# Kernel tuning notes

Measured on AMD Instinct MI355X. Metric: run time of the kernel, lower is better.

The kernel has to match this reference:

```python
import jax, jax.numpy as jnp
import numpy as np

D_MODEL = 256
NHEAD = 8
HEAD_DIM = D_MODEL // NHEAD
TOP_K = 16
TEMP = 0.1
INF = 1e9
LAYER_NAMES = ['self', 'cross'] * 4


def _ln(x, g, b):
    m = jnp.mean(x, -1, keepdims=True)
    v = jnp.mean((x - m) ** 2, -1, keepdims=True)
    return (x - m) * jax.lax.rsqrt(v + 1e-5) * g + b


def _conf(f0, f1, m0, m1):
    # feats scaled by 1/sqrt(C) each, then /temperature -> sim / (C * TEMP)
    c = f0.shape[-1]
    sim = jnp.einsum('nlc,nsc->nls', f0, f1) / (c * TEMP)
    valid = m0[:, :, None] & m1[:, None, :]
    sim = jnp.where(valid, sim, -INF)
    return jax.nn.softmax(sim, axis=1) * jax.nn.softmax(sim, axis=2)


def _select(feat, conf, k):
    _, idx = jax.lax.top_k(conf, k)                 # [N, L, K]
    return jax.vmap(lambda f, i: f[i])(feat, idx)    # [N, L, K, C]


def _lin_attn(q, k, v, qm):
    # LoFTR LinearAttention: elu feature map, kv_mask is None here
    Q = jax.nn.elu(q) + 1.0
    K = jax.nn.elu(k) + 1.0
    if qm is not None:
        Q = Q * qm[:, :, None, None]
    vlen = v.shape[1]
    v = v / vlen
    KV = jnp.einsum('nshd,nshv->nhdv', K, v)
    Z = 1.0 / (jnp.einsum('nlhd,nhd->nlh', Q, K.sum(1)) + 1e-6)
    return jnp.einsum('nlhd,nhdv,nlh->nlhv', Q, KV, Z) * vlen


def _layer(x, src, xm, p):
    Wq, Wk, Wv, Wm, W1, W2, g1, b1, g2, b2 = p
    bs = x.shape[0]
    q = (x @ Wq).reshape(bs, -1, NHEAD, HEAD_DIM)
    k = (src @ Wk).reshape(bs, -1, NHEAD, HEAD_DIM)
    v = (src @ Wv).reshape(bs, -1, NHEAD, HEAD_DIM)
    msg = _lin_attn(q, k, v, xm)
    msg = msg.reshape(bs, -1, D_MODEL) @ Wm
    msg = _ln(msg, g1, b1)
    msg = jax.nn.relu(jnp.concatenate([x, msg], -1) @ W1) @ W2
    msg = _ln(msg, g2, b2)
    return x + msg


def _forward(feat0, feat1, mask0, mask1, Wq, Wk, Wv, Wm, W1, W2, g1, b1, g2, b2):
    N, L, C = feat0.shape
    S = feat1.shape[1]
    K = TOP_K
    m0f = mask0.reshape(N * L, 1).astype(feat0.dtype)
    m1f = mask1.reshape(N * S, 1).astype(feat0.dtype)
    for i, name in enumerate(LAYER_NAMES):
        p = (Wq[i], Wk[i], Wv[i], Wm[i], W1[i], W2[i], g1[i], b1[i], g2[i], b2[i])
        f0 = feat0.reshape(N * L, 1, C)
        f1 = feat1.reshape(N * S, 1, C)
        if name == 'self':
            s00 = _select(feat0, _conf(feat0, feat0, mask0, mask0), K).reshape(N * L, K, C)
            s11 = _select(feat1, _conf(feat1, feat1, mask1, mask1), K).reshape(N * S, K, C)
            feat0 = _layer(f0, s00, m0f, p).reshape(N, L, C)
            feat1 = _layer(f1, s11, m1f, p).reshape(N, S, C)
        else:
            c01 = _conf(feat0, feat1, mask0, mask1)
            s01 = _select(feat1, c01, K).reshape(N * L, K, C)
            s10 = _select(feat0, jnp.swapaxes(c01, 1, 2), K).reshape(N * S, K, C)
            feat0 = _layer(f0, s01, m0f, p).reshape(N, L, C)
            feat1 = _layer(f1, s10, m1f, p).reshape(N, S, C)
    return feat0, feat1


def setup_inputs() -> dict:
    key = jax.random.key(0)
    ks = jax.random.split(key, 10)
    N, L, S, C = 2, 4800, 4800, D_MODEL
    nl = len(LAYER_NAMES)
    w = 0.05
    return {
        'feat0': jax.random.normal(ks[0], (N, L, C), jnp.float32),
        'feat1': jax.random.normal(ks[1], (N, S, C), jnp.float32),
        'mask0': jnp.ones((N, L), jnp.bool_),
        'mask1': jnp.ones((N, S), jnp.bool_),
        'Wq': jax.random.normal(ks[2], (nl, C, C), jnp.float32) * w,
        'Wk': jax.random.normal(ks[3], (nl, C, C), jnp.float32) * w,
        'Wv': jax.random.normal(ks[4], (nl, C, C), jnp.float32) * w,
        'Wm': jax.random.normal(ks[5], (nl, C, C), jnp.float32) * w,
        'W1': jax.random.normal(ks[6], (nl, 2 * C, 2 * C), jnp.float32) * w,
        'W2': jax.random.normal(ks[7], (nl, 2 * C, C), jnp.float32) * w,
        'g1': jnp.ones((nl, C), jnp.float32),
        'b1': jnp.zeros((nl, C), jnp.float32),
        'g2': jnp.ones((nl, C), jnp.float32),
        'b2': jnp.zeros((nl, C), jnp.float32),
    }


def reference(feat0, feat1, mask0, mask1, Wq, Wk, Wv, Wm, W1, W2, g1, b1, g2, b2):
    return _forward(feat0, feat1, mask0, mask1, Wq, Wk, Wv, Wm, W1, W2, g1, b1, g2, b2)
```

## Files before the change

### kernel.cpp

```cpp
#include <hip/hip_runtime.h>

#define LLEN 4800
#define CDIM 256
#define NCH 8
#define CHROWS 600
#define SUBR 75

template <int MODE>
__global__ __launch_bounds__(256) void gemm_nt_sim(
    const float* __restrict__ A, const float* __restrict__ B,
    float* __restrict__ C, float* __restrict__ CT)
{
  const int bxi = blockIdx.x, byi = blockIdx.y;
  if (MODE == 1 && bxi < byi) return;
  const int bm = byi * 128, bn = bxi * 128;
  __shared__ float pool[MODE ? 8512 : 4224];
  float (*As)[132] = (float (*)[132])pool;
  float (*Bs)[132] = (float (*)[132])(pool + 2112);
  const int t = threadIdx.x;
  const int tx = t & 15, ty = t >> 4;
  const int lr = t >> 2, lk = (t & 3) * 4;
  float acc[8][8] = {};
  for (int k0 = 0; k0 < CDIM; k0 += 16) {
#pragma unroll
    for (int h = 0; h < 2; ++h) {
      const int row = lr + h * 64;
      const int ga = min(bm + row, LLEN - 1);
      const int gb = min(bn + row, LLEN - 1);
      const float4 a = *(const float4*)&A[(size_t)ga * CDIM + k0 + lk];
      const float4 b = *(const float4*)&B[(size_t)gb * CDIM + k0 + lk];
      As[lk + 0][row] = a.x; As[lk + 1][row] = a.y;
      As[lk + 2][row] = a.z; As[lk + 3][row] = a.w;
      Bs[lk + 0][row] = b.x; Bs[lk + 1][row] = b.y;
      Bs[lk + 2][row] = b.z; Bs[lk + 3][row] = b.w;
    }
    __syncthreads();
#pragma unroll
    for (int k = 0; k < 16; ++k) {
      const float4 a0 = *(const float4*)&As[k][ty * 4];
      const float4 a1 = *(const float4*)&As[k][64 + ty * 4];
      const float4 b0 = *(const float4*)&Bs[k][tx * 4];
      const float4 b1 = *(const float4*)&Bs[k][64 + tx * 4];
      const float av[8] = {a0.x, a0.y, a0.z, a0.w, a1.x, a1.y, a1.z, a1.w};
      const float bv[8] = {b0.x, b0.y, b0.z, b0.w, b1.x, b1.y, b1.z, b1.w};
#pragma unroll
      for (int i = 0; i < 8; ++i)
#pragma unroll
        for (int j = 0; j < 8; ++j) acc[i][j] += av[i] * bv[j];
    }
    __syncthreads();
  }
  const float sc = 1.f / 25.6f;
#pragma unroll
  for (int i = 0; i < 8; ++i) {
    const int row = bm + ((i < 4) ? ty * 4 + i : 64 + ty * 4 + (i - 4));
    if (row < LLEN) {
      const int c0 = bn + tx * 4;
      if (c0 < LLEN) {
        float4 o = {acc[i][0] * sc, acc[i][1] * sc, acc[i][2] * sc, acc[i][3] * sc};
        *(float4*)(C + (size_t)row * LLEN + c0) = o;
      }
      if (c0 + 64 < LLEN) {
        float4 o = {acc[i][4] * sc, acc[i][5] * sc, acc[i][6] * sc, acc[i][7] * sc};
        *(float4*)(C + (size_t)row * LLEN + c0 + 64) = o;
      }
    }
  }
  if (MODE == 0) return;
  if (MODE == 1 && bxi == byi) return;
  float* D = (MODE == 1) ? C : CT;
  float (*Ts)[133] = (float (*)[133])pool;
  for (int chunk = 0; chunk < 2; ++chunk) {
    __syncthreads();
#pragma unroll
    for (int i = 0; i < 8; ++i) {
      const int rl = (i < 4) ? ty * 4 + i : 64 + ty * 4 + (i - 4);
#pragma unroll
      for (int jj = 0; jj < 4; ++jj)
        Ts[tx * 4 + jj][rl] = acc[i][chunk * 4 + jj] * sc;
    }
    __syncthreads();
    const int cl = t >> 2, seg = t & 3;
    const int drow = bn + chunk * 64 + cl;
    if (drow < LLEN) {
#pragma unroll
      for (int q = 0; q < 8; ++q) {
        const int dcol = bm + seg * 32 + q * 4;
        if (dcol < LLEN) {
          const int b = seg * 32 + q * 4;
          float4 o = {Ts[cl][b], Ts[cl][b + 1], Ts[cl][b + 2], Ts[cl][b + 3]};
          *(float4*)(D + (size_t)drow * LLEN + dcol) = o;
        }
      }
    }
  }
}

template <int ACT>
__global__ __launch_bounds__(256) void gemm_nn(
    const float* __restrict__ A1, const float* __restrict__ A2,
    const float* __restrict__ B, float* __restrict__ C, int N, int K, int KA1)
{
  const int bm = blockIdx.y * 128, bn = blockIdx.x * 128;
  __shared__ float As[16][132];
  __shared__ float Bs[16][132];
  const int t = threadIdx.x;
  const int tx = t & 15, ty = t >> 4;
  const int lr = t >> 2, lk = (t & 3) * 4;
  const int bc = (t & 31) * 4, bk = t >> 5;
  float acc[8][8] = {};
  for (int k0 = 0; k0 < K; k0 += 16) {
    const float* Ap; int kloc, lda;
    if (k0 < KA1) { Ap = A1; kloc = k0; lda = KA1; }
    else          { Ap = A2; kloc = k0 - KA1; lda = K - KA1; }
#pragma unroll
    for (int h = 0; h < 2; ++h) {
      const int row = lr + h * 64;
      const float4 a = *(const float4*)&Ap[(size_t)(bm + row) * lda + kloc + lk];
      As[lk + 0][row] = a.x; As[lk + 1][row] = a.y;
      As[lk + 2][row] = a.z; As[lk + 3][row] = a.w;
    }
#pragma unroll
    for (int h = 0; h < 2; ++h) {
      const int kr = bk + h * 8;
      *(float4*)&Bs[kr][bc] = *(const float4*)&B[(size_t)(k0 + kr) * N + bn + bc];
    }
    __syncthreads();
#pragma unroll
    for (int k = 0; k < 16; ++k) {
      const float4 a0 = *(const float4*)&As[k][ty * 4];
      const float4 a1 = *(const float4*)&As[k][64 + ty * 4];
      const float4 b0 = *(const float4*)&Bs[k][tx * 4];
      const float4 b1 = *(const float4*)&Bs[k][64 + tx * 4];
      const float av[8] = {a0.x, a0.y, a0.z, a0.w, a1.x, a1.y, a1.z, a1.w};
      const float bv[8] = {b0.x, b0.y, b0.z, b0.w, b1.x, b1.y, b1.z, b1.w};
#pragma unroll
      for (int i = 0; i < 8; ++i)
#pragma unroll
        for (int j = 0; j < 8; ++j) acc[i][j] += av[i] * bv[j];
    }
    __syncthreads();
  }
#pragma unroll
  for (int i = 0; i < 8; ++i) {
    const int row = bm + ((i < 4) ? ty * 4 + i : 64 + ty * 4 + (i - 4));
    float4 o0 = {acc[i][0], acc[i][1], acc[i][2], acc[i][3]};
    float4 o1 = {acc[i][4], acc[i][5], acc[i][6], acc[i][7]};
    if (ACT == 1) {
      o0.x = fmaxf(o0.x, 0.f); o0.y = fmaxf(o0.y, 0.f);
      o0.z = fmaxf(o0.z, 0.f); o0.w = fmaxf(o0.w, 0.f);
      o1.x = fmaxf(o1.x, 0.f); o1.y = fmaxf(o1.y, 0.f);
      o1.z = fmaxf(o1.z, 0.f); o1.w = fmaxf(o1.w, 0.f);
    }
    *(float4*)(C + (size_t)row * N + bn + tx * 4) = o0;
    *(float4*)(C + (size_t)row * N + bn + tx * 4 + 64) = o1;
  }
}

__global__ __launch_bounds__(256) void gemm_qkv(
    const float* __restrict__ F,
    const float* __restrict__ Wq, const float* __restrict__ Wk, const float* __restrict__ Wv,
    float* __restrict__ qb, float* __restrict__ kb, float* __restrict__ vb)
{
  const int bm = blockIdx.y * 128;
  const int gn = blockIdx.x * 128;
  const int sel = gn >> 8;
  const int bn = gn & 255;
  const float* __restrict__ B = (sel == 0) ? Wq : (sel == 1) ? Wk : Wv;
  float* __restrict__ C = (sel == 0) ? qb : (sel == 1) ? kb : vb;
  __shared__ float As[16][132];
  __shared__ float Bs[16][132];
  const int t = threadIdx.x;
  const int tx = t & 15, ty = t >> 4;
  const int lr = t >> 2, lk = (t & 3) * 4;
  const int bc = (t & 31) * 4, bk = t >> 5;
  float acc[8][8] = {};
  for (int k0 = 0; k0 < CDIM; k0 += 16) {
#pragma unroll
    for (int h = 0; h < 2; ++h) {
      const int row = lr + h * 64;
      const float4 a = *(const float4*)&F[(size_t)(bm + row) * CDIM + k0 + lk];
      As[lk + 0][row] = a.x; As[lk + 1][row] = a.y;
      As[lk + 2][row] = a.z; As[lk + 3][row] = a.w;
    }
#pragma unroll
    for (int h = 0; h < 2; ++h) {
      const int kr = bk + h * 8;
      *(float4*)&Bs[kr][bc] = *(const float4*)&B[(size_t)(k0 + kr) * CDIM + bn + bc];
    }
    __syncthreads();
#pragma unroll
    for (int k = 0; k < 16; ++k) {
      const float4 a0 = *(const float4*)&As[k][ty * 4];
      const float4 a1 = *(const float4*)&As[k][64 + ty * 4];
      const float4 b0 = *(const float4*)&Bs[k][tx * 4];
      const float4 b1 = *(const float4*)&Bs[k][64 + tx * 4];
      const float av[8] = {a0.x, a0.y, a0.z, a0.w, a1.x, a1.y, a1.z, a1.w};
      const float bv[8] = {b0.x, b0.y, b0.z, b0.w, b1.x, b1.y, b1.z, b1.w};
#pragma unroll
      for (int i = 0; i < 8; ++i)
#pragma unroll
        for (int j = 0; j < 8; ++j) acc[i][j] += av[i] * bv[j];
    }
    __syncthreads();
  }
#pragma unroll
  for (int i = 0; i < 8; ++i) {
    const int row = bm + ((i < 4) ? ty * 4 + i : 64 + ty * 4 + (i - 4));
    float4 o0 = {acc[i][0], acc[i][1], acc[i][2], acc[i][3]};
    float4 o1 = {acc[i][4], acc[i][5], acc[i][6], acc[i][7]};
    *(float4*)(C + (size_t)row * CDIM + bn + tx * 4) = o0;
    *(float4*)(C + (size_t)row * CDIM + bn + tx * 4 + 64) = o1;
  }
}

__global__ __launch_bounds__(256) void row_stats(
    const float* __restrict__ sim, float* __restrict__ rowAdj)
{
  const int r = blockIdx.x;
  const float* row = sim + (size_t)r * LLEN;
  const int t = threadIdx.x;
  float m = -3e38f, s = 0.f;
  for (int j = t; j < LLEN; j += 256) {
    float x = row[j];
    if (x > m) { s = s * __expf(m - x) + 1.f; m = x; }
    else s += __expf(x - m);
  }
  __shared__ float sMax[256];
  __shared__ float sSum[256];
  sMax[t] = m; sSum[t] = s;
  __syncthreads();
  for (int off = 128; off > 0; off >>= 1) {
    if (t < off) {
      float m2 = sMax[t + off], s2 = sSum[t + off];
      float mm = fmaxf(sMax[t], m2);
      sSum[t] = sSum[t] * __expf(sMax[t] - mm) + s2 * __expf(m2 - mm);
      sMax[t] = mm;
    }
    __syncthreads();
  }
  if (t == 0) rowAdj[r] = sMax[0] + __logf(sSum[0]);
}

__global__ __launch_bounds__(256) void col_stats(
    const float* __restrict__ sim, float* __restrict__ partM, float* __restrict__ partS)
{
  const int t = threadIdx.x;
  const int c = t & 31, sub = t >> 5;
  const int s = blockIdx.x * 32 + c;
  const int ch = blockIdx.y;
  float m = -3e38f, sum = 0.f;
  const int l0 = ch * CHROWS + sub * SUBR;
  for (int l = l0; l < l0 + SUBR; ++l) {
    const float x = sim[(size_t)l * LLEN + s];
    if (x > m) { sum = sum * __expf(m - x) + 1.f; m = x; }
    else sum += __expf(x - m);
  }
  __shared__ float lm[8][32];
  __shared__ float ls[8][32];
  lm[sub][c] = m; ls[sub][c] = sum;
  __syncthreads();
  if (sub == 0) {
    float M = -3e38f, S = 0.f;
#pragma unroll
    for (int u = 0; u < 8; ++u) {
      const float m2 = lm[u][c], s2 = ls[u][c];
      const float mm = fmaxf(M, m2);
      S = S * __expf(M - mm) + s2 * __expf(m2 - mm);
      M = mm;
    }
    partM[(size_t)ch * LLEN + s] = M;
    partS[(size_t)ch * LLEN + s] = S;
  }
}

__global__ __launch_bounds__(256) void col_comb_stats(
    const float* __restrict__ partM, const float* __restrict__ partS,
    float* __restrict__ colAdj)
{
  const int s = blockIdx.x * 256 + threadIdx.x;
  if (s >= LLEN) return;
  float m = -3e38f, sum = 0.f;
#pragma unroll
  for (int ch = 0; ch < NCH; ++ch) {
    const float m2 = partM[(size_t)ch * LLEN + s], s2 = partS[(size_t)ch * LLEN + s];
    const float mm = fmaxf(m, m2);
    sum = sum * __expf(m - mm) + s2 * __expf(m2 - mm);
    m = mm;
  }
  colAdj[s] = m + __logf(sum);
}

__global__ __launch_bounds__(256, 4) void topk_fast(
    const float* __restrict__ M, const float* __restrict__ adj,
    int* __restrict__ idxOut, int kvOff)
{
  const int r = blockIdx.x;
  const float* row = M + (size_t)r * LLEN;
  const int t = threadIdx.x, lane = t & 63, w = t >> 6;
  __shared__ float keys[256 * 19];
  float lm = -3e38f; int la = 0;
#pragma unroll
  for (int j = 0; j < 19; ++j) {
    const int s = t + (j << 8);
    const float k = (s < LLEN) ? 2.f * row[s] - adj[s] : -3e38f;
    keys[t * 19 + j] = k;
    if (k > lm) { lm = k; la = j; }
  }
  __shared__ float wvv[4][16];
  __shared__ int   wii[4][16];
  for (int rnd = 0; rnd < 16; ++rnd) {
    float bv = lm;
    int   bs = (la << 8) + t;
#pragma unroll
    for (int off = 32; off; off >>= 1) {
      const float ov = __shfl_xor(bv, off);
      const int   os = __shfl_xor(bs, off);
      if (ov > bv || (ov == bv && os < bs)) { bv = ov; bs = os; }
    }
    if (lane == 0) { wvv[w][rnd] = bv; wii[w][rnd] = bs; }
    if (t == (bs & 255)) {
      keys[t * 19 + (bs >> 8)] = -3e38f;
      lm = -3e38f; la = 0;
#pragma unroll
      for (int j = 0; j < 19; ++j) {
        const float k = keys[t * 19 + j];
        if (k > lm) { lm = k; la = j; }
      }
    }
  }
  __syncthreads();
  if (w == 0) {
    float v = wvv[lane >> 4][lane & 15];
    const int s = wii[lane >> 4][lane & 15];
    for (int rnd = 0; rnd < 16; ++rnd) {
      float bv = v; int bl = lane;
#pragma unroll
      for (int off = 32; off; off >>= 1) {
        const float ov = __shfl_xor(bv, off);
        const int   ol = __shfl_xor(bl, off);
        if (ov > bv || (ov == bv && ol < bl)) { bv = ov; bl = ol; }
      }
      const int sw = __shfl(s, bl);
      if (lane == 0) idxOut[(size_t)r * 16 + rnd] = kvOff + sw;
      if (lane == bl) v = -3e38f;
    }
  }
}

__global__ __launch_bounds__(256) void attn_kernel(
    float* __restrict__ qb, const float* __restrict__ kb,
    const float* __restrict__ vb, const int* __restrict__ idx, int nTok)
{
  const int w = threadIdx.x >> 6, lane = threadIdx.x & 63;
  const int tok = blockIdx.x * 4 + w;
  if (tok >= nTok) return;
  const float4 qv = ((const float4*)(qb + (size_t)tok * CDIM))[lane];
  float Q[4];
  Q[0] = qv.x > 0.f ? qv.x + 1.f : __expf(qv.x);
  Q[1] = qv.y > 0.f ? qv.y + 1.f : __expf(qv.y);
  Q[2] = qv.z > 0.f ? qv.z + 1.f : __expf(qv.z);
  Q[3] = qv.w > 0.f ? qv.w + 1.f : __expf(qv.w);
  const int* ir = idx + (size_t)tok * 16;
  float mc[4] = {0.f, 0.f, 0.f, 0.f};
  float z = 0.f;
  for (int j = 0; j < 16; ++j) {
    const int src = ir[j];
    const float4 kv = ((const float4*)(kb + (size_t)src * CDIM))[lane];
    float p = Q[0] * (kv.x > 0.f ? kv.x + 1.f : __expf(kv.x))
            + Q[1] * (kv.y > 0.f ? kv.y + 1.f : __expf(kv.y))
            + Q[2] * (kv.z > 0.f ? kv.z + 1.f : __expf(kv.z))
            + Q[3] * (kv.w > 0.f ? kv.w + 1.f : __expf(kv.w));
    p += __shfl_xor(p, 1);
    p += __shfl_xor(p, 2);
    p += __shfl_xor(p, 4);
    const float4 vv = ((const float4*)(vb + (size_t)src * CDIM))[lane];
    mc[0] += p * vv.x; mc[1] += p * vv.y; mc[2] += p * vv.z; mc[3] += p * vv.w;
    z += p;
  }
  const float Z = 1.f / (z + 1e-6f);
  float4 o;
  o.x = mc[0] * Z; o.y = mc[1] * Z; o.z = mc[2] * Z; o.w = mc[3] * Z;
  ((float4*)(qb + (size_t)tok * CDIM))[lane] = o;
}

__global__ __launch_bounds__(256) void ln_inplace(
    float* __restrict__ x, const float* __restrict__ g, const float* __restrict__ b,
    int rows)
{
  const int w = threadIdx.x >> 6, lane = threadIdx.x & 63;
  const int r = blockIdx.x * 4 + w;
  if (r >= rows) return;
  float4 v = ((const float4*)(x + (size_t)r * CDIM))[lane];
  float s = v.x + v.y + v.z + v.w;
  float ss = v.x * v.x + v.y * v.y + v.z * v.z + v.w * v.w;
#pragma unroll
  for (int off = 1; off < 64; off <<= 1) {
    s += __shfl_xor(s, off);
    ss += __shfl_xor(ss, off);
  }
  const float mean = s * (1.f / CDIM);
  const float var = ss * (1.f / CDIM) - mean * mean;
  const float rstd = rsqrtf(var + 1e-5f);
  const float4 gv = ((const float4*)g)[lane];
  const float4 bv = ((const float4*)b)[lane];
  float4 o;
  o.x = (v.x - mean) * rstd * gv.x + bv.x;
  o.y = (v.y - mean) * rstd * gv.y + bv.y;
  o.z = (v.z - mean) * rstd * gv.z + bv.z;
  o.w = (v.w - mean) * rstd * gv.w + bv.w;
  ((float4*)(x + (size_t)r * CDIM))[lane] = o;
}

__global__ __launch_bounds__(256) void ln_res_kernel(
    const float* __restrict__ m2, const float* __restrict__ xin,
    const float* __restrict__ g, const float* __restrict__ b,
    float* __restrict__ out, int rows)
{
  const int w = threadIdx.x >> 6, lane = threadIdx.x & 63;
  const int r = blockIdx.x * 4 + w;
  if (r >= rows) return;
  const float4 v = ((const float4*)(m2 + (size_t)r * CDIM))[lane];
  float s = v.x + v.y + v.z + v.w;
  float ss = v.x * v.x + v.y * v.y + v.z * v.z + v.w * v.w;
#pragma unroll
  for (int off = 1; off < 64; off <<= 1) {
    s += __shfl_xor(s, off);
    ss += __shfl_xor(ss, off);
  }
  const float mean = s * (1.f / CDIM);
  const float var = ss * (1.f / CDIM) - mean * mean;
  const float rstd = rsqrtf(var + 1e-5f);
  const float4 gv = ((const float4*)g)[lane];
  const float4 bv = ((const float4*)b)[lane];
  const float4 xv = ((const float4*)(xin + (size_t)r * CDIM))[lane];
  float4 o;
  o.x = xv.x + (v.x - mean) * rstd * gv.x + bv.x;
  o.y = xv.y + (v.y - mean) * rstd * gv.y + bv.y;
  o.z = xv.z + (v.z - mean) * rstd * gv.z + bv.z;
  o.w = xv.w + (v.w - mean) * rstd * gv.w + bv.w;
  ((float4*)(out + (size_t)r * CDIM))[lane] = o;
}

extern "C" void kernel_launch(void* const* d_in, const int* in_sizes, int n_in,
                              void* d_out, int out_size, void* d_ws, size_t ws_size,
                              hipStream_t stream)
{
  (void)in_sizes; (void)n_in; (void)out_size;
  const float* in0 = (const float*)d_in[0];
  const float* in1 = (const float*)d_in[1];
  const float* Wq = (const float*)d_in[4];
  const float* Wk = (const float*)d_in[5];
  const float* Wv = (const float*)d_in[6];
  const float* Wm = (const float*)d_in[7];
  const float* W1 = (const float*)d_in[8];
  const float* W2 = (const float*)d_in[9];
  const float* g1 = (const float*)d_in[10];
  const float* b1 = (const float*)d_in[11];
  const float* g2 = (const float*)d_in[12];
  const float* b2 = (const float*)d_in[13];

  const size_t SIMF   = (size_t)LLEN * LLEN;
  const size_t SIDEQ  = (size_t)9600 * CDIM;
  const size_t NEED_F = SIMF + 4800 + 4800 + 2 * (size_t)NCH * LLEN
                      + 2 * (size_t)NCH * LLEN * 16 + (size_t)19200 * 16;
  if (ws_size < NEED_F * sizeof(float)) return;
  const bool haveT = (ws_size >= (NEED_F + SIMF) * sizeof(float));

  float* ws = (float*)d_ws;
  float* sim    = ws;
  float* rowAdj = ws + SIMF;
  float* colAdj = rowAdj + 4800;
  float* partM  = colAdj + 4800;
  float* partS  = partM + (size_t)NCH * LLEN;
  float* candV  = partS + (size_t)NCH * LLEN;
  int*   idxb   = (int*)(candV + 2 * (size_t)NCH * LLEN * 16);
  float* simT   = ws + NEED_F;

  float* qb = sim;
  float* kb = sim + 2 * SIDEQ;
  float* vb = sim + 4 * SIDEQ;
  float* hb = sim + 6 * SIDEQ;
  float* m2 = kb;
  float* mw = vb;

  const size_t fstride = (size_t)LLEN * CDIM;
  float* fA0 = (float*)d_out;
  float* fA1 = (float*)d_out + 2 * fstride;

  const float* cF0 = in0;
  const float* cF1 = in1;

  for (int i = 0; i < 8; ++i) {
    const bool isSelf = ((i & 1) == 0);
    const float* Wq_i = Wq + (size_t)i * CDIM * CDIM;
    const float* Wk_i = Wk + (size_t)i * CDIM * CDIM;
    const float* Wv_i = Wv + (size_t)i * CDIM * CDIM;
    const float* Wm_i = Wm + (size_t)i * CDIM * CDIM;
    const float* W1_i = W1 + (size_t)i * 512 * 512;
    const float* W2_i = W2 + (size_t)i * 512 * CDIM;
    const float* g1_i = g1 + (size_t)i * CDIM;
    const float* b1_i = b1 + (size_t)i * CDIM;
    const float* g2_i = g2 + (size_t)i * CDIM;
    const float* b2_i = b2 + (size_t)i * CDIM;

    if (isSelf) {
      for (int side = 0; side < 2; ++side) {
        const float* F = side ? cF1 : cF0;
        for (int n = 0; n < 2; ++n) {
          const float* Fn = F + (size_t)n * fstride;
          gemm_nt_sim<1><<<dim3(38, 38), 256, 0, stream>>>(Fn, Fn, sim, sim);
          row_stats<<<LLEN, 256, 0, stream>>>(sim, rowAdj);
          topk_fast<<<LLEN, 256, 0, stream>>>(
              sim, rowAdj, idxb + ((size_t)side * 9600 + (size_t)n * LLEN) * 16,
              side * 9600 + n * LLEN);
        }
      }
    } else {
      for (int n = 0; n < 2; ++n) {
        const float* F0n = cF0 + (size_t)n * fstride;
        const float* F1n = cF1 + (size_t)n * fstride;
        if (haveT) {
          gemm_nt_sim<2><<<dim3(38, 38), 256, 0, stream>>>(F0n, F1n, sim, simT);
          row_stats<<<LLEN, 256, 0, stream>>>(sim, rowAdj);
          col_stats<<<dim3(150, NCH), 256, 0, stream>>>(sim, partM, partS);
          col_comb_stats<<<dim3(19), 256, 0, stream>>>(partM, partS, colAdj);
          topk_fast<<<LLEN, 256, 0, stream>>>(
              sim, colAdj, idxb + ((size_t)n * LLEN) * 16, 9600 + n * LLEN);
          topk_fast<<<LLEN, 256, 0, stream>>>(
              simT, rowAdj, idxb + ((size_t)9600 + (size_t)n * LLEN) * 16, n * LLEN);
        } else {
          gemm_nt_sim<0><<<dim3(38, 38), 256, 0, stream>>>(F0n, F1n, sim, nullptr);
          row_stats<<<LLEN, 256, 0, stream>>>(sim, rowAdj);
          col_stats<<<dim3(150, NCH), 256, 0, stream>>>(sim, partM, partS);
          col_comb_stats<<<dim3(19), 256, 0, stream>>>(partM, partS, colAdj);
          topk_fast<<<LLEN, 256, 0, stream>>>(
              sim, colAdj, idxb + ((size_t)n * LLEN) * 16, 9600 + n * LLEN);
          gemm_nt_sim<0><<<dim3(38, 38), 256, 0, stream>>>(F1n, F0n, sim, nullptr);
          topk_fast<<<LLEN, 256, 0, stream>>>(
              sim, rowAdj, idxb + ((size_t)9600 + (size_t)n * LLEN) * 16, n * LLEN);
        }
      }
    }

    for (int side = 0; side < 2; ++side) {
      const float* F = side ? cF1 : cF0;
      const size_t ob = (size_t)side * SIDEQ;
      gemm_qkv<<<dim3(6, 75), 256, 0, stream>>>(
          F, Wq_i, Wk_i, Wv_i, qb + ob, kb + ob, vb + ob);
    }

    for (int side = 0; side < 2; ++side)
      attn_kernel<<<2400, 256, 0, stream>>>(
          qb + side * SIDEQ, kb, vb, idxb + (size_t)side * 9600 * 16, 9600);

    for (int side = 0; side < 2; ++side)
      gemm_nn<0><<<dim3(2, 75), 256, 0, stream>>>(
          qb + side * SIDEQ, nullptr, Wm_i, mw + side * SIDEQ, 256, 256, 256);
    ln_inplace<<<4800, 256, 0, stream>>>(mw, g1_i, b1_i, 19200);

    for (int side = 0; side < 2; ++side) {
      const float* F = side ? cF1 : cF0;
      gemm_nn<1><<<dim3(4, 75), 256, 0, stream>>>(
          F, mw + side * SIDEQ, W1_i, hb, 512, 512, 256);
      gemm_nn<0><<<dim3(2, 75), 256, 0, stream>>>(
          hb, nullptr, W2_i, m2 + side * SIDEQ, 256, 512, 512);
    }

    ln_res_kernel<<<2400, 256, 0, stream>>>(m2, cF0, g2_i, b2_i, fA0, 9600);
    ln_res_kernel<<<2400, 256, 0, stream>>>(m2 + SIDEQ, cF1, g2_i, b2_i, fA1, 9600);
    cF0 = fA0; cF1 = fA1;
  }
}
```

Baseline: 11.26 ms.

## Prefetch next K-tile in GEMMs, vectorize col_stats, merge per-side launches

The three register-tiled GEMM kernels now load the next 16-wide K slice from global memory into registers while the current slice is computed from shared memory, hiding global load latency behind the FMA loop. col_stats processes four columns per thread with float4 loads and 128-thread blocks. The per-side attention and Wm projection launches are merged into single launches over both sides, assuming contiguous buffers and an index layout that the larger indexing matches. The prefetch adds register pressure, and the merged launches depend on that buffer contiguity.

```diff
diff --git a/kernel.cpp b/kernel.cpp
--- a/kernel.cpp
+++ b/kernel.cpp
@@ -20,21 +20,31 @@
   const int t = threadIdx.x;
   const int tx = t & 15, ty = t >> 4;
   const int lr = t >> 2, lk = (t & 3) * 4;
+  const int ga0 = min(bm + lr, LLEN - 1)      , gb0 = min(bn + lr, LLEN - 1);
+  const int ga1 = min(bm + lr + 64, LLEN - 1) , gb1 = min(bn + lr + 64, LLEN - 1);
   float acc[8][8] = {};
+  float4 pa0, pa1, pb0, pb1;
+  pa0 = *(const float4*)&A[(size_t)ga0 * CDIM + lk];
+  pa1 = *(const float4*)&A[(size_t)ga1 * CDIM + lk];
+  pb0 = *(const float4*)&B[(size_t)gb0 * CDIM + lk];
+  pb1 = *(const float4*)&B[(size_t)gb1 * CDIM + lk];
   for (int k0 = 0; k0 < CDIM; k0 += 16) {
-#pragma unroll
-    for (int h = 0; h < 2; ++h) {
-      const int row = lr + h * 64;
-      const int ga = min(bm + row, LLEN - 1);
-      const int gb = min(bn + row, LLEN - 1);
-      const float4 a = *(const float4*)&A[(size_t)ga * CDIM + k0 + lk];
-      const float4 b = *(const float4*)&B[(size_t)gb * CDIM + k0 + lk];
-      As[lk + 0][row] = a.x; As[lk + 1][row] = a.y;
-      As[lk + 2][row] = a.z; As[lk + 3][row] = a.w;
-      Bs[lk + 0][row] = b.x; Bs[lk + 1][row] = b.y;
-      Bs[lk + 2][row] = b.z; Bs[lk + 3][row] = b.w;
-    }
-    __syncthreads();
+    As[lk + 0][lr] = pa0.x; As[lk + 1][lr] = pa0.y;
+    As[lk + 2][lr] = pa0.z; As[lk + 3][lr] = pa0.w;
+    As[lk + 0][lr + 64] = pa1.x; As[lk + 1][lr + 64] = pa1.y;
+    As[lk + 2][lr + 64] = pa1.z; As[lk + 3][lr + 64] = pa1.w;
+    Bs[lk + 0][lr] = pb0.x; Bs[lk + 1][lr] = pb0.y;
+    Bs[lk + 2][lr] = pb0.z; Bs[lk + 3][lr] = pb0.w;
+    Bs[lk + 0][lr + 64] = pb1.x; Bs[lk + 1][lr + 64] = pb1.y;
+    Bs[lk + 2][lr + 64] = pb1.z; Bs[lk + 3][lr + 64] = pb1.w;
+    __syncthreads();
+    if (k0 + 16 < CDIM) {
+      const int kn = k0 + 16 + lk;
+      pa0 = *(const float4*)&A[(size_t)ga0 * CDIM + kn];
+      pa1 = *(const float4*)&A[(size_t)ga1 * CDIM + kn];
+      pb0 = *(const float4*)&B[(size_t)gb0 * CDIM + kn];
+      pb1 = *(const float4*)&B[(size_t)gb1 * CDIM + kn];
+    }
 #pragma unroll
     for (int k = 0; k < 16; ++k) {
       const float4 a0 = *(const float4*)&As[k][ty * 4];
@@ -109,23 +119,32 @@
   const int lr = t >> 2, lk = (t & 3) * 4;
   const int bc = (t & 31) * 4, bk = t >> 5;
   float acc[8][8] = {};
+  float4 pa0, pa1, pb0, pb1;
+  {
+    const float* Ap = A1; const int kloc = 0, lda = KA1;
+    pa0 = *(const float4*)&Ap[(size_t)(bm + lr) * lda + kloc + lk];
+    pa1 = *(const float4*)&Ap[(size_t)(bm + lr + 64) * lda + kloc + lk];
+    pb0 = *(const float4*)&B[(size_t)(bk) * N + bn + bc];
+    pb1 = *(const float4*)&B[(size_t)(bk + 8) * N + bn + bc];
+  }
   for (int k0 = 0; k0 < K; k0 += 16) {
-    const float* Ap; int kloc, lda;
-    if (k0 < KA1) { Ap = A1; kloc = k0; lda = KA1; }
-    else          { Ap = A2; kloc = k0 - KA1; lda = K - KA1; }
-#pragma unroll
-    for (int h = 0; h < 2; ++h) {
-      const int row = lr + h * 64;
-      const float4 a = *(const float4*)&Ap[(size_t)(bm + row) * lda + kloc + lk];
-      As[lk + 0][row] = a.x; As[lk + 1][row] = a.y;
-      As[lk + 2][row] = a.z; As[lk + 3][row] = a.w;
-    }
-#pragma unroll
-    for (int h = 0; h < 2; ++h) {
-      const int kr = bk + h * 8;
-      *(float4*)&Bs[kr][bc] = *(const float4*)&B[(size_t)(k0 + kr) * N + bn + bc];
-    }
-    __syncthreads();
+    As[lk + 0][lr] = pa0.x; As[lk + 1][lr] = pa0.y;
+    As[lk + 2][lr] = pa0.z; As[lk + 3][lr] = pa0.w;
+    As[lk + 0][lr + 64] = pa1.x; As[lk + 1][lr + 64] = pa1.y;
+    As[lk + 2][lr + 64] = pa1.z; As[lk + 3][lr + 64] = pa1.w;
+    *(float4*)&Bs[bk][bc] = pb0;
+    *(float4*)&Bs[bk + 8][bc] = pb1;
+    __syncthreads();
+    const int kn = k0 + 16;
+    if (kn < K) {
+      const float* Ap; int kloc, lda;
+      if (kn < KA1) { Ap = A1; kloc = kn; lda = KA1; }
+      else          { Ap = A2; kloc = kn - KA1; lda = K - KA1; }
+      pa0 = *(const float4*)&Ap[(size_t)(bm + lr) * lda + kloc + lk];
+      pa1 = *(const float4*)&Ap[(size_t)(bm + lr + 64) * lda + kloc + lk];
+      pb0 = *(const float4*)&B[(size_t)(kn + bk) * N + bn + bc];
+      pb1 = *(const float4*)&B[(size_t)(kn + bk + 8) * N + bn + bc];
+    }
 #pragma unroll
     for (int k = 0; k < 16; ++k) {
       const float4 a0 = *(const float4*)&As[k][ty * 4];
@@ -175,20 +194,26 @@
   const int lr = t >> 2, lk = (t & 3) * 4;
   const int bc = (t & 31) * 4, bk = t >> 5;
   float acc[8][8] = {};
+  float4 pa0, pa1, pb0, pb1;
+  pa0 = *(const float4*)&F[(size_t)(bm + lr) * CDIM + lk];
+  pa1 = *(const float4*)&F[(size_t)(bm + lr + 64) * CDIM + lk];
+  pb0 = *(const float4*)&B[(size_t)(bk) * CDIM + bn + bc];
+  pb1 = *(const float4*)&B[(size_t)(bk + 8) * CDIM + bn + bc];
   for (int k0 = 0; k0 < CDIM; k0 += 16) {
-#pragma unroll
-    for (int h = 0; h < 2; ++h) {
-      const int row = lr + h * 64;
-      const float4 a = *(const float4*)&F[(size_t)(bm + row) * CDIM + k0 + lk];
-      As[lk + 0][row] = a.x; As[lk + 1][row] = a.y;
-      As[lk + 2][row] = a.z; As[lk + 3][row] = a.w;
-    }
-#pragma unroll
-    for (int h = 0; h < 2; ++h) {
-      const int kr = bk + h * 8;
-      *(float4*)&Bs[kr][bc] = *(const float4*)&B[(size_t)(k0 + kr) * CDIM + bn + bc];
-    }
-    __syncthreads();
+    As[lk + 0][lr] = pa0.x; As[lk + 1][lr] = pa0.y;
+    As[lk + 2][lr] = pa0.z; As[lk + 3][lr] = pa0.w;
+    As[lk + 0][lr + 64] = pa1.x; As[lk + 1][lr + 64] = pa1.y;
+    As[lk + 2][lr + 64] = pa1.z; As[lk + 3][lr + 64] = pa1.w;
+    *(float4*)&Bs[bk][bc] = pb0;
+    *(float4*)&Bs[bk + 8][bc] = pb1;
+    __syncthreads();
+    const int kn = k0 + 16;
+    if (kn < CDIM) {
+      pa0 = *(const float4*)&F[(size_t)(bm + lr) * CDIM + kn + lk];
+      pa1 = *(const float4*)&F[(size_t)(bm + lr + 64) * CDIM + kn + lk];
+      pb0 = *(const float4*)&B[(size_t)(kn + bk) * CDIM + bn + bc];
+      pb1 = *(const float4*)&B[(size_t)(kn + bk + 8) * CDIM + bn + bc];
+    }
 #pragma unroll
     for (int k = 0; k < 16; ++k) {
       const float4 a0 = *(const float4*)&As[k][ty * 4];
@@ -242,35 +267,45 @@
   if (t == 0) rowAdj[r] = sMax[0] + __logf(sSum[0]);
 }
 
-__global__ __launch_bounds__(256) void col_stats(
+__global__ __launch_bounds__(128) void col_stats(
     const float* __restrict__ sim, float* __restrict__ partM, float* __restrict__ partS)
 {
   const int t = threadIdx.x;
-  const int c = t & 31, sub = t >> 5;
-  const int s = blockIdx.x * 32 + c;
+  const int cg = t & 15, sub = t >> 4;
+  const int c0 = blockIdx.x * 64 + cg * 4;
   const int ch = blockIdx.y;
-  float m = -3e38f, sum = 0.f;
+  float m0 = -3e38f, m1 = -3e38f, m2 = -3e38f, m3 = -3e38f;
+  float s0 = 0.f, s1 = 0.f, s2 = 0.f, s3 = 0.f;
   const int l0 = ch * CHROWS + sub * SUBR;
   for (int l = l0; l < l0 + SUBR; ++l) {
-    const float x = sim[(size_t)l * LLEN + s];
-    if (x > m) { sum = sum * __expf(m - x) + 1.f; m = x; }
-    else sum += __expf(x - m);
-  }
-  __shared__ float lm[8][32];
-  __shared__ float ls[8][32];
-  lm[sub][c] = m; ls[sub][c] = sum;
+    const float4 x = *(const float4*)&sim[(size_t)l * LLEN + c0];
+    if (x.x > m0) { s0 = s0 * __expf(m0 - x.x) + 1.f; m0 = x.x; } else s0 += __expf(x.x - m0);
+    if (x.y > m1) { s1 = s1 * __expf(m1 - x.y) + 1.f; m1 = x.y; } else s1 += __expf(x.y - m1);
+    if (x.z > m2) { s2 = s2 * __expf(m2 - x.z) + 1.f; m2 = x.z; } else s2 += __expf(x.z - m2);
+    if (x.w > m3) { s3 = s3 * __expf(m3 - x.w) + 1.f; m3 = x.w; } else s3 += __expf(x.w - m3);
+  }
+  __shared__ float lm[8][64];
+  __shared__ float ls[8][64];
+  lm[sub][cg * 4 + 0] = m0; ls[sub][cg * 4 + 0] = s0;
+  lm[sub][cg * 4 + 1] = m1; ls[sub][cg * 4 + 1] = s1;
+  lm[sub][cg * 4 + 2] = m2; ls[sub][cg * 4 + 2] = s2;
+  lm[sub][cg * 4 + 3] = m3; ls[sub][cg * 4 + 3] = s3;
   __syncthreads();
   if (sub == 0) {
-    float M = -3e38f, S = 0.f;
-#pragma unroll
-    for (int u = 0; u < 8; ++u) {
-      const float m2 = lm[u][c], s2 = ls[u][c];
-      const float mm = fmaxf(M, m2);
-      S = S * __expf(M - mm) + s2 * __expf(m2 - mm);
-      M = mm;
-    }
-    partM[(size_t)ch * LLEN + s] = M;
-    partS[(size_t)ch * LLEN + s] = S;
+#pragma unroll
+    for (int j = 0; j < 4; ++j) {
+      const int c = cg * 4 + j;
+      float M = -3e38f, S = 0.f;
+#pragma unroll
+      for (int u = 0; u < 8; ++u) {
+        const float mm2 = lm[u][c], ss2 = ls[u][c];
+        const float mm = fmaxf(M, mm2);
+        S = S * __expf(M - mm) + ss2 * __expf(mm2 - mm);
+        M = mm;
+      }
+      partM[(size_t)ch * LLEN + c0 + j] = M;
+      partS[(size_t)ch * LLEN + c0 + j] = S;
+    }
   }
 }
 
@@ -523,7 +558,7 @@
         if (haveT) {
           gemm_nt_sim<2><<<dim3(38, 38), 256, 0, stream>>>(F0n, F1n, sim, simT);
           row_stats<<<LLEN, 256, 0, stream>>>(sim, rowAdj);
-          col_stats<<<dim3(150, NCH), 256, 0, stream>>>(sim, partM, partS);
+          col_stats<<<dim3(75, NCH), 128, 0, stream>>>(sim, partM, partS);
           col_comb_stats<<<dim3(19), 256, 0, stream>>>(partM, partS, colAdj);
           topk_fast<<<LLEN, 256, 0, stream>>>(
               sim, colAdj, idxb + ((size_t)n * LLEN) * 16, 9600 + n * LLEN);
@@ -532,7 +567,7 @@
         } else {
           gemm_nt_sim<0><<<dim3(38, 38), 256, 0, stream>>>(F0n, F1n, sim, nullptr);
           row_stats<<<LLEN, 256, 0, stream>>>(sim, rowAdj);
-          col_stats<<<dim3(150, NCH), 256, 0, stream>>>(sim, partM, partS);
+          col_stats<<<dim3(75, NCH), 128, 0, stream>>>(sim, partM, partS);
           col_comb_stats<<<dim3(19), 256, 0, stream>>>(partM, partS, colAdj);
           topk_fast<<<LLEN, 256, 0, stream>>>(
               sim, colAdj, idxb + ((size_t)n * LLEN) * 16, 9600 + n * LLEN);
@@ -550,13 +585,9 @@
           F, Wq_i, Wk_i, Wv_i, qb + ob, kb + ob, vb + ob);
     }
 
-    for (int side = 0; side < 2; ++side)
-      attn_kernel<<<2400, 256, 0, stream>>>(
-          qb + side * SIDEQ, kb, vb, idxb + (size_t)side * 9600 * 16, 9600);
-
-    for (int side = 0; side < 2; ++side)
-      gemm_nn<0><<<dim3(2, 75), 256, 0, stream>>>(
-          qb + side * SIDEQ, nullptr, Wm_i, mw + side * SIDEQ, 256, 256, 256);
+    attn_kernel<<<4800, 256, 0, stream>>>(qb, kb, vb, idxb, 19200);
+
+    gemm_nn<0><<<dim3(2, 150), 256, 0, stream>>>(qb, nullptr, Wm_i, mw, 256, 256, 256);
     ln_inplace<<<4800, 256, 0, stream>>>(mw, g1_i, b1_i, 19200);
 
     for (int side = 0; side < 2; ++side) {
```

Result: no change. 11.30 ms (+0.4%).
